# Optimization experiments

Hardware: AMD Instinct MI355X
Metric: run time of the kernel (lower is better)

The kernel has to match this reference:

```python
import jax, jax.numpy as jnp
import numpy as np

PHI = 1.6
JITTER = 1e-4
ETA = 1.0
BETA = 0.5
EPS_CHOL = 1e-6
R_NEIGH = 2


def _solve3(L, d):
    # lower-triangular 3x3 forward substitution; L broadcasts against d[..., 3]
    y0 = d[..., 0] / L[..., 0, 0]
    y1 = (d[..., 1] - L[..., 1, 0] * y0) / L[..., 1, 1]
    y2 = (d[..., 2] - L[..., 2, 0] * y0 - L[..., 2, 1] * y1) / L[..., 2, 2]
    return jnp.stack([y0, y1, y2], axis=-1)


def _overlap_score(delta, L):
    # fused_gaussian_overlap_score: Gaussian log-overlap ~ -0.5*(Mahalanobis + logdet)
    y = _solve3(L, delta)
    maha = jnp.sum(y * y, axis=-1)
    logdet = 2.0 * jnp.sum(jnp.log(jnp.diagonal(L, axis1=-2, axis2=-1)), axis=-1)
    return -0.5 * (maha + logdet)


def _head(x, ln_g, ln_b, W1, b1, W2, b2):
    # LayerNorm -> Linear -> SiLU -> Linear(->1), squeeze
    m = jnp.mean(x, axis=-1, keepdims=True)
    v = jnp.var(x, axis=-1, keepdims=True)
    h = (x - m) / jnp.sqrt(v + 1e-5) * ln_g + ln_b
    h = jax.nn.silu(h @ W1 + b1)
    return (h @ W2 + b2)[..., 0]


def setup_inputs() -> dict:
    key = jax.random.key(0)
    ks = jax.random.split(key, 12)
    B, Kp, M, C = 2, 1024, 8, 256
    s_parent = jax.random.normal(ks[0], (B, Kp, C), jnp.float32)
    mu_p = jax.random.normal(ks[1], (B, Kp, 3), jnp.float32) * 10.0
    A = jax.random.normal(ks[2], (B, Kp, 3, 3), jnp.float32) * 0.5
    Sigma_p = jnp.einsum('bkij,bklj->bkil', A, A) + 0.05 * jnp.eye(3, dtype=jnp.float32)
    mask_parent = jnp.ones((B, Kp), jnp.float32)
    xi_noise = jax.random.normal(ks[3], (B, Kp, M, 3), jnp.float32)
    emb = jax.random.normal(ks[4], (M, C), jnp.float32) * 0.02
    lin = lambda k, fi, fo, s=0.02: jax.random.normal(k, (fi, fo), jnp.float32) * s
    return dict(
        s_parent=s_parent, mu_p=mu_p, Sigma_p=Sigma_p, mask_parent=mask_parent,
        xi_noise=xi_noise, emb=emb,
        gate_ln_g=jnp.ones((C,), jnp.float32), gate_ln_b=jnp.zeros((C,), jnp.float32),
        gate_W1=lin(ks[5], C, C), gate_b1=jnp.zeros((C,), jnp.float32),
        gate_W2=lin(ks[6], C, 1), gate_b2=jnp.zeros((1,), jnp.float32),
        prior_ln_g=jnp.ones((C,), jnp.float32), prior_ln_b=jnp.zeros((C,), jnp.float32),
        prior_W1=lin(ks[7], C, C), prior_b1=jnp.zeros((C,), jnp.float32),
        prior_W2=lin(ks[8], C, 1), prior_b2=jnp.zeros((1,), jnp.float32),
        geom_W=lin(ks[9], C, 3, 0.01), geom_b=jnp.zeros((3,), jnp.float32),
        K_target=6144,
    )


def reference(s_parent, mu_p, Sigma_p, mask_parent, xi_noise, emb,
              gate_ln_g, gate_ln_b, gate_W1, gate_b1, gate_W2, gate_b2,
              prior_ln_g, prior_ln_b, prior_W1, prior_b1, prior_W2, prior_b2,
              geom_W, geom_b, K_target):
    B, Kp, C = s_parent.shape
    M = emb.shape[0]
    Kc = Kp * M
    I3 = jnp.eye(3, dtype=s_parent.dtype)

    # --- candidate children from per-parent Cholesky splat ---
    Lp = jnp.linalg.cholesky(Sigma_p + EPS_CHOL * I3)               # [B,Kp,3,3]
    xi = xi_noise + (emb @ geom_W + geom_b)                          # [B,Kp,M,3]
    mu0 = mu_p[:, :, None, :] + jnp.einsum('bkae,bkme->bkma', Lp, xi)
    mu0 = mu0.reshape(B, Kc, 3)

    j0 = jnp.repeat(jnp.arange(Kp), M)                               # [Kc] birth parent
    t_ids = jnp.tile(jnp.arange(M), Kp)                              # [Kc] child slot
    m0 = mask_parent[:, j0]

    # --- gate g ---
    gate_in = s_parent[:, j0, :] + emb[t_ids]                        # [B,Kc,C]
    b = _head(gate_in, gate_ln_g, gate_ln_b, gate_W1, gate_b1, gate_W2, gate_b2)
    a = jax.nn.softplus(_head(s_parent, prior_ln_g, prior_ln_b, prior_W1, prior_b1, prior_W2, prior_b2))
    b = b + BETA * jnp.log(a[:, j0] + 1e-8)
    g = jax.nn.sigmoid(b / max(ETA, 1e-6)) * m0                      # [B,Kc]
    loss_count = jnp.mean((jnp.sum(g, axis=1) - float(K_target)) ** 2)

    # --- top-R neighbor parents by overlap score (indices only, no grad) ---
    mu0_birth = mu_p[:, j0, :]                                       # mu of birth parent
    delta1 = mu0_birth[:, :, None, :] - mu_p[:, None, :, :]          # [B,Kc,Kp,3]
    score1 = _overlap_score(delta1, Lp[:, None])                     # [B,Kc,Kp]
    self_hot = (jnp.arange(Kp)[None, :] == j0[:, None])              # [Kc,Kp]
    score1 = jnp.where(self_hot[None], 1e9, score1)
    _, neigh = jax.lax.top_k(jax.lax.stop_gradient(score1), R_NEIGH) # [B,Kc,R], col0=j0

    bidx = jnp.arange(B)[:, None, None]
    mu_nei = mu_p[bidx, neigh]                                       # [B,Kc,R,3]
    Sig_nei = Sigma_p[bidx, neigh]                                   # [B,Kc,R,3,3]
    L_nei = Lp[bidx, neigh]
    s_nei = s_parent[bidx, neigh]                                    # [B,Kc,R,C]

    # --- soft responsibilities over the R neighbors ---
    score2 = _overlap_score(mu0[:, :, None, :] - mu_nei, L_nei)      # [B,Kc,R]
    w = jax.nn.softmax(score2, axis=-1)

    # --- moment-matching refine (sparse form of B_resp: rows of B are w scattered at neigh) ---
    mu_child = jnp.einsum('bir,bird->bid', w, mu_nei)                # [B,Kc,3]
    intra = jnp.einsum('bir,birmn->bimn', w, Sig_nei) * PHI ** (-2)
    dmu = mu_nei - mu_child[:, :, None, :]
    inter = jnp.einsum('bir,birm,birn->bimn', w, dmu, dmu)
    Sigma_child = intra + inter + JITTER * I3                        # [B,Kc,3,3]

    s_mix = jnp.einsum('bir,birc->bic', w, s_nei)
    s_child0 = g[..., None] * s_mix                                  # [B,Kc,C]
    return s_child0, mu_child, Sigma_child, g, loss_count
```

## Files before the change

### kernel.cpp

```cpp
#include <hip/hip_runtime.h>
#include <math.h>

#define NPAR 2048
#define KP   1024
#define MM   8
#define CC   256
#define KC   8192
#define NCH  16384

#define WS_PKL    0
#define WS_PKI    8192
#define WS_PKM    16384
#define WS_L22    24576
#define WS_MEANSP 26624
#define WS_SUMSQ  28672
#define WS_DOT8   30720
#define WS_APRIOR 47104
#define WS_EGATE  49152
#define WS_UGATE  51200
#define WS_C0GATE 51456
#define WS_GEO    51712
#define WS_MEANE  51736
#define WS_SUMSQE 51744
#define WS_NEIGH  51752
#define WS_PGATE  53824
#define WS_GPART  578112

#define OUT_S    0
#define OUT_MU   4194304
#define OUT_SIG  4243456
#define OUT_G    4390912
#define OUT_LOSS 4407296

__device__ __forceinline__ float siluf(float x){ return x / (1.f + expf(-x)); }
__device__ __forceinline__ float softplusf(float x){ return x > 20.f ? x : log1pf(expf(x)); }

__global__ __launch_bounds__(256) void kA(const float* __restrict__ sp,
                                          const float* __restrict__ mu_p,
                                          const float* __restrict__ Sig,
                                          const float* __restrict__ emb,
                                          const float* __restrict__ geom_W,
                                          const float* __restrict__ geom_b,
                                          const float* __restrict__ g_ln_g,
                                          const float* __restrict__ g_ln_b,
                                          const float* __restrict__ gW1,
                                          const float* __restrict__ gb1,
                                          const float* __restrict__ p_ln_g,
                                          const float* __restrict__ p_ln_b,
                                          const float* __restrict__ pW1,
                                          const float* __restrict__ pb1,
                                          const float* __restrict__ pW2,
                                          const float* __restrict__ pb2,
                                          float* __restrict__ ws) {
  __shared__ float smem[10 * 1024];
  int blk = blockIdx.x;
  int t = threadIdx.x;

  if (blk < 512) {
    int b = blk >> 8;
#pragma unroll
    for (int q = 0; q < 4; q++) {
      int loc = q * 256 + t;
      int pid = b * KP + loc;
      const float* S = Sig + pid * 9;
      float a00 = S[0] + 1e-6f, a10 = S[3], a11 = S[4] + 1e-6f;
      float a20 = S[6], a21 = S[7], a22 = S[8] + 1e-6f;
      float L00 = sqrtf(a00); float i0 = 1.f / L00;
      float L10 = a10 * i0, L20 = a20 * i0;
      float L11 = sqrtf(a11 - L10 * L10); float i1 = 1.f / L11;
      float L21 = (a21 - L20 * L10) * i1;
      float L22 = sqrtf(a22 - L20 * L20 - L21 * L21); float i2 = 1.f / L22;
      float logdet = 2.f * logf(L00 * L11 * L22);
      float mx = mu_p[pid * 3 + 0], my = mu_p[pid * 3 + 1], mz = mu_p[pid * 3 + 2];
      smem[0 * 1024 + loc] = L10;
      smem[1 * 1024 + loc] = L20;
      smem[2 * 1024 + loc] = L21;
      smem[3 * 1024 + loc] = logdet;
      smem[4 * 1024 + loc] = i0;
      smem[5 * 1024 + loc] = i1;
      smem[6 * 1024 + loc] = i2;
      smem[7 * 1024 + loc] = mx;
      smem[8 * 1024 + loc] = my;
      smem[9 * 1024 + loc] = mz;
      if ((loc >> 2) == (blk & 255)) {
        float4 pkl = {L10, L20, L21, logdet};
        float4 pki = {i0, i1, i2, L00};
        float4 pkm = {mx, my, mz, L11};
        *(float4*)(ws + WS_PKL + pid * 4) = pkl;
        *(float4*)(ws + WS_PKI + pid * 4) = pki;
        *(float4*)(ws + WS_PKM + pid * 4) = pkm;
        ws[WS_L22 + pid] = L22;
      }
    }
    __syncthreads();

    int wv = blk * 4 + (t >> 6);
    int lane = t & 63;
    int j = wv & (KP - 1);
    float qx = smem[7 * 1024 + j], qy = smem[8 * 1024 + j], qz = smem[9 * 1024 + j];
    float best = -3.4e38f; int bidx = 1 << 30;
    for (int it = 0; it < 16; it++) {
      int k = it * 64 + lane;
      float dx = qx - smem[7 * 1024 + k];
      float dy = qy - smem[8 * 1024 + k];
      float dz = qz - smem[9 * 1024 + k];
      float y0 = dx * smem[4 * 1024 + k];
      float y1 = (dy - smem[0 * 1024 + k] * y0) * smem[5 * 1024 + k];
      float y2 = (dz - smem[1 * 1024 + k] * y0 - smem[2 * 1024 + k] * y1) * smem[6 * 1024 + k];
      float sc = -0.5f * (y0 * y0 + y1 * y1 + y2 * y2 + smem[3 * 1024 + k]);
      if (k == j) sc = -3.4e38f;
      if (sc > best || (sc == best && k < bidx)) { best = sc; bidx = k; }
    }
#pragma unroll
    for (int o = 32; o > 0; o >>= 1) {
      float ob = __shfl_xor(best, o);
      int   oi = __shfl_xor(bidx, o);
      if (ob > best || (ob == best && oi < bidx)) { best = ob; bidx = oi; }
    }
    if (lane == 0) ((int*)ws)[WS_NEIGH + wv] = bidx;
  } else {
    float (*xs)[256] = (float(*)[256])smem;
    float* statred   = smem + 2048;
    float (*redS)[8] = (float(*)[8])(smem + 2432);
    float (*redQ)[8] = (float(*)[8])(smem + 2464);
    float (*mv)[8]   = (float(*)[8])(smem + 2496);
    float (*red)[8]  = (float(*)[8])(smem + 2528);

    int cblk = blk - 512;
    bool prior = (cblk >= 256 && cblk < 512);
    const float* W1 = prior ? pW1 : gW1;

    if (cblk < 256) {
      int base = cblk * 8;
      float g = g_ln_g[t];
      float vr[8], em[8];
#pragma unroll
      for (int r = 0; r < 8; r++) vr[r] = sp[(base + r) * 256 + t];
#pragma unroll
      for (int m = 0; m < 8; m++) em[m] = emb[m * 256 + t];
#pragma unroll
      for (int r = 0; r < 8; r++) xs[r][t] = vr[r] * g;
      int wave = t >> 6, lane = t & 63;
#pragma unroll
      for (int r = 0; r < 8; r++) {
        float p0 = vr[r], p1 = vr[r] * vr[r];
        float d[8];
#pragma unroll
        for (int m = 0; m < 8; m++) d[m] = vr[r] * em[m];
#pragma unroll
        for (int o = 32; o > 0; o >>= 1) {
          p0 += __shfl_xor(p0, o);
          p1 += __shfl_xor(p1, o);
#pragma unroll
          for (int m = 0; m < 8; m++) d[m] += __shfl_xor(d[m], o);
        }
        if (lane == 0) {
          float* dst = statred + (wave * 8 + r) * 10;
          dst[0] = p0; dst[1] = p1;
#pragma unroll
          for (int m = 0; m < 8; m++) dst[2 + m] = d[m];
        }
      }
      __syncthreads();
      if (t < 8) {
        int r = t;
        float s = 0.f, ss = 0.f, dd[8] = {0, 0, 0, 0, 0, 0, 0, 0};
#pragma unroll
        for (int w = 0; w < 4; w++) {
          float* srcp = statred + (w * 8 + r) * 10;
          s += srcp[0]; ss += srcp[1];
#pragma unroll
          for (int m = 0; m < 8; m++) dd[m] += srcp[2 + m];
        }
        ws[WS_MEANSP + base + r] = s * (1.f / 256.f);
        ws[WS_SUMSQ + base + r]  = ss;
#pragma unroll
        for (int m = 0; m < 8; m++) ws[WS_DOT8 + (base + r) * 8 + m] = dd[m];
      }
    } else if (cblk < 512) {
      int base = (cblk - 256) * 8;
      float vr[8], s1[8], s2[8];
#pragma unroll
      for (int r = 0; r < 8; r++) {
        vr[r] = sp[(base + r) * 256 + t];
        s1[r] = vr[r];
        s2[r] = vr[r] * vr[r];
      }
#pragma unroll
      for (int o = 32; o > 0; o >>= 1) {
#pragma unroll
        for (int r = 0; r < 8; r++) { s1[r] += __shfl_xor(s1[r], o); s2[r] += __shfl_xor(s2[r], o); }
      }
      int wave = t >> 6;
      if ((t & 63) == 0) {
#pragma unroll
        for (int r = 0; r < 8; r++) { redS[wave][r] = s1[r]; redQ[wave][r] = s2[r]; }
      }
      __syncthreads();
      if (t < 8) {
        float sum = redS[0][t] + redS[1][t] + redS[2][t] + redS[3][t];
        float sq  = redQ[0][t] + redQ[1][t] + redQ[2][t] + redQ[3][t];
        float mean = sum * (1.f / 256.f);
        float var  = sq * (1.f / 256.f) - mean * mean;
        mv[0][t] = mean;
        mv[1][t] = rsqrtf(var + 1e-5f);
      }
      __syncthreads();
      float pg = p_ln_g[t], pbv = p_ln_b[t];
#pragma unroll
      for (int r = 0; r < 8; r++)
        xs[r][t] = (vr[r] - mv[0][r]) * mv[1][r] * pg + pbv;
    } else if (cblk == 512) {
      float g = g_ln_g[t];
#pragma unroll
      for (int r = 0; r < 8; r++) xs[r][t] = emb[r * 256 + t] * g;
    } else if (cblk == 513) {
      xs[0][t] = g_ln_g[t];
      xs[1][t] = g_ln_b[t];
#pragma unroll
      for (int r = 2; r < 8; r++) xs[r][t] = 0.f;
    } else {
      if (t < 192) {
        int o = t >> 3, lane8 = t & 7;
        int m = o / 3, d = o % 3;
        float acc = 0.f;
        for (int k = lane8; k < 256; k += 8) acc += emb[m * 256 + k] * geom_W[k * 3 + d];
        acc += __shfl_xor(acc, 1); acc += __shfl_xor(acc, 2); acc += __shfl_xor(acc, 4);
        if (lane8 == 0) ws[WS_GEO + o] = acc + geom_b[d];
      } else {
        int o = (t - 192) >> 3, lane8 = t & 7;
        if (o < 8) {
          float s = 0.f, ss = 0.f;
          for (int k = lane8; k < 256; k += 8) { float e = emb[o * 256 + k]; s += e; ss += e * e; }
          s  += __shfl_xor(s, 1);  s  += __shfl_xor(s, 2);  s  += __shfl_xor(s, 4);
          ss += __shfl_xor(ss, 1); ss += __shfl_xor(ss, 2); ss += __shfl_xor(ss, 4);
          if (lane8 == 0) { ws[WS_MEANE + o] = s * (1.f / 256.f); ws[WS_SUMSQE + o] = ss; }
        }
      }
      return;
    }
    __syncthreads();

    float acc[8] = {0, 0, 0, 0, 0, 0, 0, 0};
    for (int k4 = 0; k4 < 256; k4 += 4) {
      float w0 = W1[(k4 + 0) * 256 + t];
      float w1 = W1[(k4 + 1) * 256 + t];
      float w2 = W1[(k4 + 2) * 256 + t];
      float w3 = W1[(k4 + 3) * 256 + t];
#pragma unroll
      for (int r = 0; r < 8; r++) {
        float4 x4 = *(const float4*)&xs[r][k4];
        acc[r] += x4.x * w0 + x4.y * w1 + x4.z * w2 + x4.w * w3;
      }
    }

    if (cblk < 256) {
      int base = cblk * 8;
#pragma unroll
      for (int r = 0; r < 8; r++) ws[WS_PGATE + (base + r) * 256 + t] = acc[r];
    } else if (cblk < 512) {
      int base = (cblk - 256) * 8;
      float b1 = pb1[t], w2 = pW2[t];
      float tv[8];
#pragma unroll
      for (int r = 0; r < 8; r++) {
        float h = acc[r] + b1;
        tv[r] = siluf(h) * w2;
      }
#pragma unroll
      for (int o = 32; o > 0; o >>= 1) {
#pragma unroll
        for (int r = 0; r < 8; r++) tv[r] += __shfl_xor(tv[r], o);
      }
      int wave = t >> 6;
      if ((t & 63) == 0) {
#pragma unroll
        for (int r = 0; r < 8; r++) red[wave][r] = tv[r];
      }
      __syncthreads();
      if (t < 8) {
        float sum = red[0][t] + red[1][t] + red[2][t] + red[3][t] + pb2[0];
        ws[WS_APRIOR + base + t] = softplusf(sum);
      }
    } else if (cblk == 512) {
#pragma unroll
      for (int r = 0; r < 8; r++) ws[WS_EGATE + r * 256 + t] = acc[r];
    } else {
      ws[WS_UGATE + t]  = acc[0];
      ws[WS_C0GATE + t] = acc[1] + gb1[t];
    }
  }
}

__global__ __launch_bounds__(256) void kD(const float* __restrict__ sp,
                                          const float* __restrict__ Sig,
                                          const float* __restrict__ mask,
                                          const float* __restrict__ xi_noise,
                                          const float* __restrict__ gW2,
                                          const float* __restrict__ gb2,
                                          float* __restrict__ ws,
                                          float* __restrict__ out) {
  __shared__ float gpart[4];
  int wv   = blockIdx.x * 4 + (threadIdx.x >> 6);
  int lane = threadIdx.x & 63;
  int b = wv >> 13;
  int i = wv & (KC - 1);
  int j = i >> 3;
  int m = i & 7;
  int prow = b * KP + j;

  float mean_x = ws[WS_MEANSP + prow] + ws[WS_MEANE + m];
  float Ex2 = ws[WS_SUMSQ + prow] + 2.f * ws[WS_DOT8 + prow * 8 + m] + ws[WS_SUMSQE + m];
  float var = Ex2 * (1.f / 256.f) - mean_x * mean_x;
  float rstd = rsqrtf(var + 1e-5f);

  int c4 = lane * 4;
  float Pv[4], Ev[4], Uv[4], C0v[4], W2v[4];
  *(float4*)Pv  = *(const float4*)(ws + WS_PGATE + prow * 256 + c4);
  *(float4*)Ev  = *(const float4*)(ws + WS_EGATE + m * 256 + c4);
  *(float4*)Uv  = *(const float4*)(ws + WS_UGATE + c4);
  *(float4*)C0v = *(const float4*)(ws + WS_C0GATE + c4);
  *(float4*)W2v = *(const float4*)(gW2 + c4);
  float partial = 0.f;
#pragma unroll
  for (int q = 0; q < 4; q++) {
    float pre = (Pv[q] + Ev[q] - mean_x * Uv[q]) * rstd + C0v[q];
    partial += siluf(pre) * W2v[q];
  }
#pragma unroll
  for (int o = 32; o > 0; o >>= 1) partial += __shfl_xor(partial, o);
  float aP = ws[WS_APRIOR + prow];
  float bval = partial + gb2[0] + 0.5f * logf(aP + 1e-8f);
  float g = (1.f / (1.f + expf(-bval))) * mask[prow];

  if (lane == 0) gpart[threadIdx.x >> 6] = g;
  __syncthreads();
  if (threadIdx.x == 0)
    ws[WS_GPART + blockIdx.x] = gpart[0] + gpart[1] + gpart[2] + gpart[3];

  const float4 plP = *(const float4*)(ws + WS_PKL + prow * 4);
  const float4 piP = *(const float4*)(ws + WS_PKI + prow * 4);
  const float4 pmP = *(const float4*)(ws + WS_PKM + prow * 4);
  float L22 = ws[WS_L22 + prow];

  int xbase = (prow * 8 + m) * 3;
  float x0 = xi_noise[xbase + 0] + ws[WS_GEO + m * 3 + 0];
  float x1 = xi_noise[xbase + 1] + ws[WS_GEO + m * 3 + 1];
  float x2 = xi_noise[xbase + 2] + ws[WS_GEO + m * 3 + 2];
  float m0x = pmP.x + piP.w * x0;
  float m0y = pmP.y + plP.x * x0 + pmP.w * x1;
  float m0z = pmP.z + plP.y * x0 + plP.z * x1 + L22 * x2;

  int n1 = ((const int*)ws)[WS_NEIGH + prow];
  int nrow1 = b * KP + n1;
  const float4 plN = *(const float4*)(ws + WS_PKL + nrow1 * 4);
  const float4 piN = *(const float4*)(ws + WS_PKI + nrow1 * 4);
  const float4 pmN = *(const float4*)(ws + WS_PKM + nrow1 * 4);

  float sc[2], nx[2], ny[2], nz[2];
  {
    float dx = m0x - pmP.x, dy = m0y - pmP.y, dz = m0z - pmP.z;
    float y0 = dx * piP.x;
    float y1 = (dy - plP.x * y0) * piP.y;
    float y2 = (dz - plP.y * y0 - plP.z * y1) * piP.z;
    sc[0] = -0.5f * (y0*y0 + y1*y1 + y2*y2 + plP.w);
    nx[0] = pmP.x; ny[0] = pmP.y; nz[0] = pmP.z;
  }
  {
    float dx = m0x - pmN.x, dy = m0y - pmN.y, dz = m0z - pmN.z;
    float y0 = dx * piN.x;
    float y1 = (dy - plN.x * y0) * piN.y;
    float y2 = (dz - plN.y * y0 - plN.z * y1) * piN.z;
    sc[1] = -0.5f * (y0*y0 + y1*y1 + y2*y2 + plN.w);
    nx[1] = pmN.x; ny[1] = pmN.y; nz[1] = pmN.z;
  }
  float mxs = fmaxf(sc[0], sc[1]);
  float e0 = expf(sc[0] - mxs), e1 = expf(sc[1] - mxs);
  float inv = 1.f / (e0 + e1);
  float w0 = e0 * inv, w1 = e1 * inv;

  float mcx = w0 * nx[0] + w1 * nx[1];
  float mcy = w0 * ny[0] + w1 * ny[1];
  float mcz = w0 * nz[0] + w1 * nz[1];

  float d0x = nx[0] - mcx, d0y = ny[0] - mcy, d0z = nz[0] - mcz;
  float d1x = nx[1] - mcx, d1y = ny[1] - mcy, d1z = nz[1] - mcz;
  const float* S0 = Sig + prow * 9;
  const float* S1 = Sig + nrow1 * 9;
  const float PHIm2 = 0.390625f;
  float Sout[9];
  float dd0[3] = {d0x, d0y, d0z};
  float dd1[3] = {d1x, d1y, d1z};
#pragma unroll
  for (int a = 0; a < 3; a++)
#pragma unroll
    for (int e = 0; e < 3; e++) {
      float v = (w0 * S0[a*3+e] + w1 * S1[a*3+e]) * PHIm2
              + w0 * dd0[a] * dd0[e] + w1 * dd1[a] * dd1[e];
      if (a == e) v += 1e-4f;
      Sout[a*3+e] = v;
    }

  if (lane == 0) {
    float* om = out + OUT_MU + wv * 3;
    om[0] = mcx; om[1] = mcy; om[2] = mcz;
    out[OUT_G + wv] = g;
    float* os = out + OUT_SIG + wv * 9;
#pragma unroll
    for (int q = 0; q < 9; q++) os[q] = Sout[q];
  }

  float s0v[4], s1v[4], ov[4];
  *(float4*)s0v = *(const float4*)(sp + prow * 256 + c4);
  *(float4*)s1v = *(const float4*)(sp + nrow1 * 256 + c4);
  float gw0 = g * w0, gw1 = g * w1;
#pragma unroll
  for (int q = 0; q < 4; q++) ov[q] = gw0 * s0v[q] + gw1 * s1v[q];
  *(float4*)(out + OUT_S + wv * 256 + c4) = *(float4*)ov;
}

__global__ __launch_bounds__(256) void kF(const float* __restrict__ ws,
                                          const int* __restrict__ Kt,
                                          float* __restrict__ out) {
  __shared__ float red[4][2];
  int t = threadIdx.x;
  const float* gp = ws + WS_GPART;
  float s0 = 0.f, s1 = 0.f;
#pragma unroll
  for (int it = 0; it < 8; it++) {
    s0 += gp[it * 256 + t];
    s1 += gp[2048 + it * 256 + t];
  }
#pragma unroll
  for (int o = 32; o > 0; o >>= 1) {
    s0 += __shfl_xor(s0, o);
    s1 += __shfl_xor(s1, o);
  }
  int wave = t >> 6;
  if ((t & 63) == 0) { red[wave][0] = s0; red[wave][1] = s1; }
  __syncthreads();
  if (t == 0) {
    float S0 = red[0][0] + red[1][0] + red[2][0] + red[3][0];
    float S1 = red[0][1] + red[1][1] + red[2][1] + red[3][1];
    float K = (float)Kt[0];
    float l0 = S0 - K, l1 = S1 - K;
    out[OUT_LOSS] = 0.5f * (l0 * l0 + l1 * l1);
  }
}

extern "C" void kernel_launch(void* const* d_in, const int* in_sizes, int n_in,
                              void* d_out, int out_size, void* d_ws, size_t ws_size,
                              hipStream_t stream) {
  const float* s_parent   = (const float*)d_in[0];
  const float* mu_p       = (const float*)d_in[1];
  const float* Sigma_p    = (const float*)d_in[2];
  const float* mask_par   = (const float*)d_in[3];
  const float* xi_noise   = (const float*)d_in[4];
  const float* emb        = (const float*)d_in[5];
  const float* gate_ln_g  = (const float*)d_in[6];
  const float* gate_ln_b  = (const float*)d_in[7];
  const float* gate_W1    = (const float*)d_in[8];
  const float* gate_b1    = (const float*)d_in[9];
  const float* gate_W2    = (const float*)d_in[10];
  const float* gate_b2    = (const float*)d_in[11];
  const float* prior_ln_g = (const float*)d_in[12];
  const float* prior_ln_b = (const float*)d_in[13];
  const float* prior_W1   = (const float*)d_in[14];
  const float* prior_b1   = (const float*)d_in[15];
  const float* prior_W2   = (const float*)d_in[16];
  const float* prior_b2   = (const float*)d_in[17];
  const float* geom_W     = (const float*)d_in[18];
  const float* geom_b     = (const float*)d_in[19];
  const int*   K_target   = (const int*)d_in[20];

  float* ws  = (float*)d_ws;
  float* out = (float*)d_out;

  kA<<<1027, 256, 0, stream>>>(s_parent, mu_p, Sigma_p, emb, geom_W, geom_b,
                               gate_ln_g, gate_ln_b, gate_W1, gate_b1,
                               prior_ln_g, prior_ln_b, prior_W1, prior_b1,
                               prior_W2, prior_b2, ws);
  kD<<<NCH / 4, 256, 0, stream>>>(s_parent, Sigma_p, mask_par, xi_noise,
                                  gate_W2, gate_b2, ws, out);
  kF<<<1, 256, 0, stream>>>(ws, K_target, out);
}
```

Measured before the change: 146.1 us.

## Double rows per block in GEMM stage and process one parent per block in child kernel

Measured after the change: 148.4 us. Within noise of the previous version (+1.6%).

```diff
diff --git a/kernel.cpp b/kernel.cpp
--- a/kernel.cpp
+++ b/kernel.cpp
@@ -120,29 +120,29 @@
     if (lane == 0) ((int*)ws)[WS_NEIGH + wv] = bidx;
   } else {
     float (*xs)[256] = (float(*)[256])smem;
-    float* statred   = smem + 2048;
-    float (*redS)[8] = (float(*)[8])(smem + 2432);
-    float (*redQ)[8] = (float(*)[8])(smem + 2464);
-    float (*mv)[8]   = (float(*)[8])(smem + 2496);
-    float (*red)[8]  = (float(*)[8])(smem + 2528);
+    float* statred    = smem + 4096;
+    float (*redS)[16] = (float(*)[16])(smem + 4736);
+    float (*redQ)[16] = (float(*)[16])(smem + 4800);
+    float (*mv)[16]   = (float(*)[16])(smem + 4864);
+    float (*red)[16]  = (float(*)[16])(smem + 4896);
 
     int cblk = blk - 512;
-    bool prior = (cblk >= 256 && cblk < 512);
+    bool prior = (cblk >= 128 && cblk < 256);
     const float* W1 = prior ? pW1 : gW1;
 
-    if (cblk < 256) {
-      int base = cblk * 8;
+    if (cblk < 128) {
+      int base = cblk * 16;
       float g = g_ln_g[t];
-      float vr[8], em[8];
-#pragma unroll
-      for (int r = 0; r < 8; r++) vr[r] = sp[(base + r) * 256 + t];
+      float vr[16], em[8];
+#pragma unroll
+      for (int r = 0; r < 16; r++) vr[r] = sp[(base + r) * 256 + t];
 #pragma unroll
       for (int m = 0; m < 8; m++) em[m] = emb[m * 256 + t];
 #pragma unroll
-      for (int r = 0; r < 8; r++) xs[r][t] = vr[r] * g;
+      for (int r = 0; r < 16; r++) xs[r][t] = vr[r] * g;
       int wave = t >> 6, lane = t & 63;
 #pragma unroll
-      for (int r = 0; r < 8; r++) {
+      for (int r = 0; r < 16; r++) {
         float p0 = vr[r], p1 = vr[r] * vr[r];
         float d[8];
 #pragma unroll
@@ -155,19 +155,19 @@
           for (int m = 0; m < 8; m++) d[m] += __shfl_xor(d[m], o);
         }
         if (lane == 0) {
-          float* dst = statred + (wave * 8 + r) * 10;
+          float* dst = statred + (wave * 16 + r) * 10;
           dst[0] = p0; dst[1] = p1;
 #pragma unroll
           for (int m = 0; m < 8; m++) dst[2 + m] = d[m];
         }
       }
       __syncthreads();
-      if (t < 8) {
+      if (t < 16) {
         int r = t;
         float s = 0.f, ss = 0.f, dd[8] = {0, 0, 0, 0, 0, 0, 0, 0};
 #pragma unroll
         for (int w = 0; w < 4; w++) {
-          float* srcp = statred + (w * 8 + r) * 10;
+          float* srcp = statred + (w * 16 + r) * 10;
           s += srcp[0]; ss += srcp[1];
 #pragma unroll
           for (int m = 0; m < 8; m++) dd[m] += srcp[2 + m];
@@ -177,11 +177,11 @@
 #pragma unroll
         for (int m = 0; m < 8; m++) ws[WS_DOT8 + (base + r) * 8 + m] = dd[m];
       }
-    } else if (cblk < 512) {
-      int base = (cblk - 256) * 8;
-      float vr[8], s1[8], s2[8];
-#pragma unroll
-      for (int r = 0; r < 8; r++) {
+    } else if (cblk < 256) {
+      int base = (cblk - 128) * 16;
+      float vr[16], s1[16], s2[16];
+#pragma unroll
+      for (int r = 0; r < 16; r++) {
         vr[r] = sp[(base + r) * 256 + t];
         s1[r] = vr[r];
         s2[r] = vr[r] * vr[r];
@@ -189,15 +189,15 @@
 #pragma unroll
       for (int o = 32; o > 0; o >>= 1) {
 #pragma unroll
-        for (int r = 0; r < 8; r++) { s1[r] += __shfl_xor(s1[r], o); s2[r] += __shfl_xor(s2[r], o); }
+        for (int r = 0; r < 16; r++) { s1[r] += __shfl_xor(s1[r], o); s2[r] += __shfl_xor(s2[r], o); }
       }
       int wave = t >> 6;
       if ((t & 63) == 0) {
 #pragma unroll
-        for (int r = 0; r < 8; r++) { redS[wave][r] = s1[r]; redQ[wave][r] = s2[r]; }
+        for (int r = 0; r < 16; r++) { redS[wave][r] = s1[r]; redQ[wave][r] = s2[r]; }
       }
       __syncthreads();
-      if (t < 8) {
+      if (t < 16) {
         float sum = redS[0][t] + redS[1][t] + redS[2][t] + redS[3][t];
         float sq  = redQ[0][t] + redQ[1][t] + redQ[2][t] + redQ[3][t];
         float mean = sum * (1.f / 256.f);
@@ -208,17 +208,19 @@
       __syncthreads();
       float pg = p_ln_g[t], pbv = p_ln_b[t];
 #pragma unroll
-      for (int r = 0; r < 8; r++)
+      for (int r = 0; r < 16; r++)
         xs[r][t] = (vr[r] - mv[0][r]) * mv[1][r] * pg + pbv;
-    } else if (cblk == 512) {
+    } else if (cblk == 256) {
       float g = g_ln_g[t];
 #pragma unroll
-      for (int r = 0; r < 8; r++) xs[r][t] = emb[r * 256 + t] * g;
-    } else if (cblk == 513) {
+      for (int r = 0; r < 8; r++)  xs[r][t] = emb[r * 256 + t] * g;
+#pragma unroll
+      for (int r = 8; r < 16; r++) xs[r][t] = 0.f;
+    } else if (cblk == 257) {
       xs[0][t] = g_ln_g[t];
       xs[1][t] = g_ln_b[t];
 #pragma unroll
-      for (int r = 2; r < 8; r++) xs[r][t] = 0.f;
+      for (int r = 2; r < 16; r++) xs[r][t] = 0.f;
     } else {
       if (t < 192) {
         int o = t >> 3, lane8 = t & 7;
@@ -241,48 +243,50 @@
     }
     __syncthreads();
 
-    float acc[8] = {0, 0, 0, 0, 0, 0, 0, 0};
+    float acc[16];
+#pragma unroll
+    for (int r = 0; r < 16; r++) acc[r] = 0.f;
     for (int k4 = 0; k4 < 256; k4 += 4) {
       float w0 = W1[(k4 + 0) * 256 + t];
       float w1 = W1[(k4 + 1) * 256 + t];
       float w2 = W1[(k4 + 2) * 256 + t];
       float w3 = W1[(k4 + 3) * 256 + t];
 #pragma unroll
-      for (int r = 0; r < 8; r++) {
+      for (int r = 0; r < 16; r++) {
         float4 x4 = *(const float4*)&xs[r][k4];
         acc[r] += x4.x * w0 + x4.y * w1 + x4.z * w2 + x4.w * w3;
       }
     }
 
-    if (cblk < 256) {
-      int base = cblk * 8;
-#pragma unroll
-      for (int r = 0; r < 8; r++) ws[WS_PGATE + (base + r) * 256 + t] = acc[r];
-    } else if (cblk < 512) {
-      int base = (cblk - 256) * 8;
+    if (cblk < 128) {
+      int base = cblk * 16;
+#pragma unroll
+      for (int r = 0; r < 16; r++) ws[WS_PGATE + (base + r) * 256 + t] = acc[r];
+    } else if (cblk < 256) {
+      int base = (cblk - 128) * 16;
       float b1 = pb1[t], w2 = pW2[t];
-      float tv[8];
-#pragma unroll
-      for (int r = 0; r < 8; r++) {
+      float tv[16];
+#pragma unroll
+      for (int r = 0; r < 16; r++) {
         float h = acc[r] + b1;
         tv[r] = siluf(h) * w2;
       }
 #pragma unroll
       for (int o = 32; o > 0; o >>= 1) {
 #pragma unroll
-        for (int r = 0; r < 8; r++) tv[r] += __shfl_xor(tv[r], o);
+        for (int r = 0; r < 16; r++) tv[r] += __shfl_xor(tv[r], o);
       }
       int wave = t >> 6;
       if ((t & 63) == 0) {
 #pragma unroll
-        for (int r = 0; r < 8; r++) red[wave][r] = tv[r];
+        for (int r = 0; r < 16; r++) red[wave][r] = tv[r];
       }
       __syncthreads();
-      if (t < 8) {
+      if (t < 16) {
         float sum = red[0][t] + red[1][t] + red[2][t] + red[3][t] + pb2[0];
         ws[WS_APRIOR + base + t] = softplusf(sum);
       }
-    } else if (cblk == 512) {
+    } else if (cblk == 256) {
 #pragma unroll
       for (int r = 0; r < 8; r++) ws[WS_EGATE + r * 256 + t] = acc[r];
     } else {
@@ -300,123 +304,136 @@
                                           const float* __restrict__ gb2,
                                           float* __restrict__ ws,
                                           float* __restrict__ out) {
-  __shared__ float gpart[4];
-  int wv   = blockIdx.x * 4 + (threadIdx.x >> 6);
+  __shared__ float gpart[8];
+  int prow = blockIdx.x;
+  int wave = threadIdx.x >> 6;
   int lane = threadIdx.x & 63;
-  int b = wv >> 13;
-  int i = wv & (KC - 1);
-  int j = i >> 3;
-  int m = i & 7;
-  int prow = b * KP + j;
-
-  float mean_x = ws[WS_MEANSP + prow] + ws[WS_MEANE + m];
-  float Ex2 = ws[WS_SUMSQ + prow] + 2.f * ws[WS_DOT8 + prow * 8 + m] + ws[WS_SUMSQE + m];
-  float var = Ex2 * (1.f / 256.f) - mean_x * mean_x;
-  float rstd = rsqrtf(var + 1e-5f);
-
+  int b = prow >> 10;
   int c4 = lane * 4;
-  float Pv[4], Ev[4], Uv[4], C0v[4], W2v[4];
-  *(float4*)Pv  = *(const float4*)(ws + WS_PGATE + prow * 256 + c4);
-  *(float4*)Ev  = *(const float4*)(ws + WS_EGATE + m * 256 + c4);
-  *(float4*)Uv  = *(const float4*)(ws + WS_UGATE + c4);
-  *(float4*)C0v = *(const float4*)(ws + WS_C0GATE + c4);
-  *(float4*)W2v = *(const float4*)(gW2 + c4);
-  float partial = 0.f;
-#pragma unroll
-  for (int q = 0; q < 4; q++) {
-    float pre = (Pv[q] + Ev[q] - mean_x * Uv[q]) * rstd + C0v[q];
-    partial += siluf(pre) * W2v[q];
-  }
-#pragma unroll
-  for (int o = 32; o > 0; o >>= 1) partial += __shfl_xor(partial, o);
-  float aP = ws[WS_APRIOR + prow];
-  float bval = partial + gb2[0] + 0.5f * logf(aP + 1e-8f);
-  float g = (1.f / (1.f + expf(-bval))) * mask[prow];
-
-  if (lane == 0) gpart[threadIdx.x >> 6] = g;
-  __syncthreads();
-  if (threadIdx.x == 0)
-    ws[WS_GPART + blockIdx.x] = gpart[0] + gpart[1] + gpart[2] + gpart[3];
+
+  float mean_sp = ws[WS_MEANSP + prow];
+  float sumsq   = ws[WS_SUMSQ + prow];
+  float aP      = ws[WS_APRIOR + prow];
+  float lgA     = gb2[0] + 0.5f * logf(aP + 1e-8f);
+  float mk      = mask[prow];
 
   const float4 plP = *(const float4*)(ws + WS_PKL + prow * 4);
   const float4 piP = *(const float4*)(ws + WS_PKI + prow * 4);
   const float4 pmP = *(const float4*)(ws + WS_PKM + prow * 4);
   float L22 = ws[WS_L22 + prow];
 
-  int xbase = (prow * 8 + m) * 3;
-  float x0 = xi_noise[xbase + 0] + ws[WS_GEO + m * 3 + 0];
-  float x1 = xi_noise[xbase + 1] + ws[WS_GEO + m * 3 + 1];
-  float x2 = xi_noise[xbase + 2] + ws[WS_GEO + m * 3 + 2];
-  float m0x = pmP.x + piP.w * x0;
-  float m0y = pmP.y + plP.x * x0 + pmP.w * x1;
-  float m0z = pmP.z + plP.y * x0 + plP.z * x1 + L22 * x2;
-
-  int n1 = ((const int*)ws)[WS_NEIGH + prow];
+  int n1 = __builtin_amdgcn_readfirstlane(((const int*)ws)[WS_NEIGH + prow]);
   int nrow1 = b * KP + n1;
   const float4 plN = *(const float4*)(ws + WS_PKL + nrow1 * 4);
   const float4 piN = *(const float4*)(ws + WS_PKI + nrow1 * 4);
   const float4 pmN = *(const float4*)(ws + WS_PKM + nrow1 * 4);
 
-  float sc[2], nx[2], ny[2], nz[2];
-  {
-    float dx = m0x - pmP.x, dy = m0y - pmP.y, dz = m0z - pmP.z;
-    float y0 = dx * piP.x;
-    float y1 = (dy - plP.x * y0) * piP.y;
-    float y2 = (dz - plP.y * y0 - plP.z * y1) * piP.z;
-    sc[0] = -0.5f * (y0*y0 + y1*y1 + y2*y2 + plP.w);
-    nx[0] = pmP.x; ny[0] = pmP.y; nz[0] = pmP.z;
-  }
-  {
-    float dx = m0x - pmN.x, dy = m0y - pmN.y, dz = m0z - pmN.z;
-    float y0 = dx * piN.x;
-    float y1 = (dy - plN.x * y0) * piN.y;
-    float y2 = (dz - plN.y * y0 - plN.z * y1) * piN.z;
-    sc[1] = -0.5f * (y0*y0 + y1*y1 + y2*y2 + plN.w);
-    nx[1] = pmN.x; ny[1] = pmN.y; nz[1] = pmN.z;
-  }
-  float mxs = fmaxf(sc[0], sc[1]);
-  float e0 = expf(sc[0] - mxs), e1 = expf(sc[1] - mxs);
-  float inv = 1.f / (e0 + e1);
-  float w0 = e0 * inv, w1 = e1 * inv;
-
-  float mcx = w0 * nx[0] + w1 * nx[1];
-  float mcy = w0 * ny[0] + w1 * ny[1];
-  float mcz = w0 * nz[0] + w1 * nz[1];
-
-  float d0x = nx[0] - mcx, d0y = ny[0] - mcy, d0z = nz[0] - mcz;
-  float d1x = nx[1] - mcx, d1y = ny[1] - mcy, d1z = nz[1] - mcz;
+  float Pv[4], Uv[4], C0v[4], W2v[4], s0v[4], s1v[4];
+  *(float4*)Pv  = *(const float4*)(ws + WS_PGATE + prow * 256 + c4);
+  *(float4*)Uv  = *(const float4*)(ws + WS_UGATE + c4);
+  *(float4*)C0v = *(const float4*)(ws + WS_C0GATE + c4);
+  *(float4*)W2v = *(const float4*)(gW2 + c4);
+  *(float4*)s0v = *(const float4*)(sp + prow * 256 + c4);
+  *(float4*)s1v = *(const float4*)(sp + nrow1 * 256 + c4);
+
   const float* S0 = Sig + prow * 9;
   const float* S1 = Sig + nrow1 * 9;
+  float S0r[9], S1r[9];
+#pragma unroll
+  for (int q = 0; q < 9; q++) { S0r[q] = S0[q]; S1r[q] = S1[q]; }
   const float PHIm2 = 0.390625f;
-  float Sout[9];
-  float dd0[3] = {d0x, d0y, d0z};
-  float dd1[3] = {d1x, d1y, d1z};
-#pragma unroll
-  for (int a = 0; a < 3; a++)
-#pragma unroll
-    for (int e = 0; e < 3; e++) {
-      float v = (w0 * S0[a*3+e] + w1 * S1[a*3+e]) * PHIm2
-              + w0 * dd0[a] * dd0[e] + w1 * dd1[a] * dd1[e];
-      if (a == e) v += 1e-4f;
-      Sout[a*3+e] = v;
-    }
-
-  if (lane == 0) {
-    float* om = out + OUT_MU + wv * 3;
-    om[0] = mcx; om[1] = mcy; om[2] = mcz;
-    out[OUT_G + wv] = g;
-    float* os = out + OUT_SIG + wv * 9;
-#pragma unroll
-    for (int q = 0; q < 9; q++) os[q] = Sout[q];
+
+#pragma unroll
+  for (int c = 0; c < 2; c++) {
+    int m  = wave * 2 + c;
+    int wv = prow * 8 + m;
+
+    float mean_x = mean_sp + ws[WS_MEANE + m];
+    float Ex2 = sumsq + 2.f * ws[WS_DOT8 + prow * 8 + m] + ws[WS_SUMSQE + m];
+    float var = Ex2 * (1.f / 256.f) - mean_x * mean_x;
+    float rstd = rsqrtf(var + 1e-5f);
+
+    float Ev[4];
+    *(float4*)Ev = *(const float4*)(ws + WS_EGATE + m * 256 + c4);
+    float partial = 0.f;
+#pragma unroll
+    for (int q = 0; q < 4; q++) {
+      float pre = (Pv[q] + Ev[q] - mean_x * Uv[q]) * rstd + C0v[q];
+      partial += siluf(pre) * W2v[q];
+    }
+#pragma unroll
+    for (int o = 32; o > 0; o >>= 1) partial += __shfl_xor(partial, o);
+    float bval = partial + lgA;
+    float g = (1.f / (1.f + expf(-bval))) * mk;
+    if (lane == 0) gpart[m] = g;
+
+    int xbase = (prow * 8 + m) * 3;
+    float x0 = xi_noise[xbase + 0] + ws[WS_GEO + m * 3 + 0];
+    float x1 = xi_noise[xbase + 1] + ws[WS_GEO + m * 3 + 1];
+    float x2 = xi_noise[xbase + 2] + ws[WS_GEO + m * 3 + 2];
+    float m0x = pmP.x + piP.w * x0;
+    float m0y = pmP.y + plP.x * x0 + pmP.w * x1;
+    float m0z = pmP.z + plP.y * x0 + plP.z * x1 + L22 * x2;
+
+    float sc0, sc1;
+    {
+      float dx = m0x - pmP.x, dy = m0y - pmP.y, dz = m0z - pmP.z;
+      float y0 = dx * piP.x;
+      float y1 = (dy - plP.x * y0) * piP.y;
+      float y2 = (dz - plP.y * y0 - plP.z * y1) * piP.z;
+      sc0 = -0.5f * (y0*y0 + y1*y1 + y2*y2 + plP.w);
+    }
+    {
+      float dx = m0x - pmN.x, dy = m0y - pmN.y, dz = m0z - pmN.z;
+      float y0 = dx * piN.x;
+      float y1 = (dy - plN.x * y0) * piN.y;
+      float y2 = (dz - plN.y * y0 - plN.z * y1) * piN.z;
+      sc1 = -0.5f * (y0*y0 + y1*y1 + y2*y2 + plN.w);
+    }
+    float mxs = fmaxf(sc0, sc1);
+    float e0 = expf(sc0 - mxs), e1 = expf(sc1 - mxs);
+    float inv = 1.f / (e0 + e1);
+    float w0 = e0 * inv, w1 = e1 * inv;
+
+    float mcx = w0 * pmP.x + w1 * pmN.x;
+    float mcy = w0 * pmP.y + w1 * pmN.y;
+    float mcz = w0 * pmP.z + w1 * pmN.z;
+
+    float dd0[3] = {pmP.x - mcx, pmP.y - mcy, pmP.z - mcz};
+    float dd1[3] = {pmN.x - mcx, pmN.y - mcy, pmN.z - mcz};
+    float Sout[9];
+#pragma unroll
+    for (int a = 0; a < 3; a++)
+#pragma unroll
+      for (int e = 0; e < 3; e++) {
+        float v = (w0 * S0r[a*3+e] + w1 * S1r[a*3+e]) * PHIm2
+                + w0 * dd0[a] * dd0[e] + w1 * dd1[a] * dd1[e];
+        if (a == e) v += 1e-4f;
+        Sout[a*3+e] = v;
+      }
+
+    if (lane == 0) {
+      float* om = out + OUT_MU + wv * 3;
+      om[0] = mcx; om[1] = mcy; om[2] = mcz;
+      out[OUT_G + wv] = g;
+      float* os = out + OUT_SIG + wv * 9;
+#pragma unroll
+      for (int q = 0; q < 9; q++) os[q] = Sout[q];
+    }
+
+    float gw0 = g * w0, gw1 = g * w1;
+    float ov[4];
+#pragma unroll
+    for (int q = 0; q < 4; q++) ov[q] = gw0 * s0v[q] + gw1 * s1v[q];
+    *(float4*)(out + OUT_S + wv * 256 + c4) = *(float4*)ov;
   }
 
-  float s0v[4], s1v[4], ov[4];
-  *(float4*)s0v = *(const float4*)(sp + prow * 256 + c4);
-  *(float4*)s1v = *(const float4*)(sp + nrow1 * 256 + c4);
-  float gw0 = g * w0, gw1 = g * w1;
-#pragma unroll
-  for (int q = 0; q < 4; q++) ov[q] = gw0 * s0v[q] + gw1 * s1v[q];
-  *(float4*)(out + OUT_S + wv * 256 + c4) = *(float4*)ov;
+  __syncthreads();
+  if (threadIdx.x == 0) {
+    float s = gpart[0] + gpart[1] + gpart[2] + gpart[3]
+            + gpart[4] + gpart[5] + gpart[6] + gpart[7];
+    ws[WS_GPART + prow] = s;
+  }
 }
 
 __global__ __launch_bounds__(256) void kF(const float* __restrict__ ws,
@@ -427,9 +444,9 @@
   const float* gp = ws + WS_GPART;
   float s0 = 0.f, s1 = 0.f;
 #pragma unroll
-  for (int it = 0; it < 8; it++) {
+  for (int it = 0; it < 4; it++) {
     s0 += gp[it * 256 + t];
-    s1 += gp[2048 + it * 256 + t];
+    s1 += gp[1024 + it * 256 + t];
   }
 #pragma unroll
   for (int o = 32; o > 0; o >>= 1) {
@@ -476,11 +493,11 @@
   float* ws  = (float*)d_ws;
   float* out = (float*)d_out;
 
-  kA<<<1027, 256, 0, stream>>>(s_parent, mu_p, Sigma_p, emb, geom_W, geom_b,
-                               gate_ln_g, gate_ln_b, gate_W1, gate_b1,
-                               prior_ln_g, prior_ln_b, prior_W1, prior_b1,
-                               prior_W2, prior_b2, ws);
-  kD<<<NCH / 4, 256, 0, stream>>>(s_parent, Sigma_p, mask_par, xi_noise,
-                                  gate_W2, gate_b2, ws, out);
+  kA<<<771, 256, 0, stream>>>(s_parent, mu_p, Sigma_p, emb, geom_W, geom_b,
+                              gate_ln_g, gate_ln_b, gate_W1, gate_b1,
+                              prior_ln_g, prior_ln_b, prior_W1, prior_b1,
+                              prior_W2, prior_b2, ws);
+  kD<<<NPAR, 256, 0, stream>>>(s_parent, Sigma_p, mask_par, xi_noise,
+                               gate_W2, gate_b2, ws, out);
   kF<<<1, 256, 0, stream>>>(ws, K_target, out);
 }
```
